# Performance work log

Hardware: AMD Instinct MI355X
Metric: run time of the kernel (lower is better)

The kernel has to match this reference:

```python
import jax, jax.numpy as jnp
import numpy as np

N = 50000   # nodes
E = 600000  # edges
F = 128     # num_node_features
H = 128     # hidden_channels
C = 10      # num_classes
G = 64      # graphs in batch


def setup_inputs() -> dict:
    key = jax.random.key(0)
    ks = jax.random.split(key, 12)
    x = jax.random.normal(ks[0], (N, F), jnp.float32)
    edge_index = jax.random.randint(ks[1], (2, E), 0, N, dtype=jnp.int32)
    batch = jnp.sort(jax.random.randint(ks[2], (N,), 0, G, dtype=jnp.int32))
    def glorot(k, shape):
        lim = np.sqrt(6.0 / (shape[0] + shape[1])).astype(np.float32)
        return jax.random.uniform(k, shape, jnp.float32, -lim, lim)
    return {
        "x": x,
        "edge_index": edge_index,
        "batch": batch,
        "W1": glorot(ks[3], (F, H)), "b1": jnp.zeros((H,), jnp.float32),
        "W2": glorot(ks[4], (H, H)), "b2": jnp.zeros((H,), jnp.float32),
        "W3": glorot(ks[5], (H, H)), "b3": jnp.zeros((H,), jnp.float32),
        "Wl": glorot(ks[6], (H, C)), "bl": jnp.zeros((C,), jnp.float32),
    }


def reference(x, edge_index, batch, W1, b1, W2, b2, W3, b3, Wl, bl):
    # GCNConv: add self-loops, symmetric degree normalization D^-1/2 A D^-1/2
    src0, dst0 = edge_index[0], edge_index[1]
    loop = jnp.arange(N, dtype=src0.dtype)
    src = jnp.concatenate([src0, loop])
    dst = jnp.concatenate([dst0, loop])
    deg = jax.ops.segment_sum(jnp.ones_like(dst, jnp.float32), dst, num_segments=N)
    dinv = jnp.where(deg > 0, jax.lax.rsqrt(deg), 0.0)
    norm = dinv[src] * dinv[dst]  # [E+N]

    def conv(h, W, b):
        h = h @ W                                  # [N, H] transform first (PyG GCNConv)
        msg = h[src] * norm[:, None]               # gather + normalize
        return jax.ops.segment_sum(msg, dst, num_segments=N) + b  # scatter-add

    h = jax.nn.relu(conv(x, W1, b1))
    h = jax.nn.relu(conv(h, W2, b2))
    h = conv(h, W3, b3)

    # global_mean_pool over batch ids
    counts = jax.ops.segment_sum(jnp.ones((N,), jnp.float32), batch, num_segments=G)
    pooled = jax.ops.segment_sum(h, batch, num_segments=G) / jnp.maximum(counts, 1.0)[:, None]
    return pooled @ Wl + bl  # [G, C]
```

## Files before the change

kernel.cpp:

```cpp
#include <hip/hip_runtime.h>
#include <hip/hip_bf16.h>

#define NN 50000
#define EE 600000
#define FF 128
#define HH 128
#define CC 10
#define GG 64
#define SB 256
#define NBSCAN ((NN + SB - 1) / SB)

typedef unsigned int uint32;
typedef unsigned short ushort16;
typedef __attribute__((ext_vector_type(8))) short short8;
typedef __attribute__((ext_vector_type(4))) float f32x4;

__device__ __forceinline__ ushort16 f2bf(float f) {
    __hip_bfloat16 b = __float2bfloat16(f);
    return *reinterpret_cast<ushort16*>(&b);
}
__device__ __forceinline__ uint32 pack2bf(float a, float b) {
    return (uint32)f2bf(a) | ((uint32)f2bf(b) << 16);
}
__device__ __forceinline__ int q8(float f) {
    return __float2int_rn(fminf(fmaxf(f * 16.f, -127.f), 127.f)) & 255;
}

__global__ void count_deg(const int* __restrict__ dst, int* __restrict__ deg) {
    int e = blockIdx.x * blockDim.x + threadIdx.x;
    if (e < EE) atomicAdd(&deg[dst[e]], 1);
}

__global__ __launch_bounds__(SB) void scan_block(const int* __restrict__ deg,
                                                 int* __restrict__ row_ptr,
                                                 int* __restrict__ bsum,
                                                 float* __restrict__ dinv) {
    __shared__ int sm[SB];
    int t = threadIdx.x;
    int i = blockIdx.x * SB + t;
    int v = (i < NN) ? deg[i] : 0;
    if (i < NN) dinv[i] = rsqrtf((float)(v + 1));
    sm[t] = v;
    __syncthreads();
    for (int off = 1; off < SB; off <<= 1) {
        int add = (t >= off) ? sm[t - off] : 0;
        __syncthreads();
        sm[t] += add;
        __syncthreads();
    }
    if (i < NN) row_ptr[i] = sm[t] - v;
    if (t == SB - 1) bsum[blockIdx.x] = sm[t];
}

__global__ void scan_bsum(int* __restrict__ bsum, int nb) {
    __shared__ int sm[256];
    int t = threadIdx.x;
    int v = (t < nb) ? bsum[t] : 0;
    sm[t] = v;
    __syncthreads();
    for (int off = 1; off < 256; off <<= 1) {
        int add = (t >= off) ? sm[t - off] : 0;
        __syncthreads();
        sm[t] += add;
        __syncthreads();
    }
    if (t < nb) bsum[t] = sm[t] - v;
}

__global__ __launch_bounds__(SB) void scan_add_tw(int* __restrict__ row_ptr,
                                                  int* __restrict__ cursor,
                                                  const int* __restrict__ bsum,
                                                  const float* __restrict__ W1,
                                                  const float* __restrict__ W2,
                                                  const float* __restrict__ W3,
                                                  ushort16* __restrict__ T1,
                                                  ushort16* __restrict__ T2,
                                                  ushort16* __restrict__ T3) {
    int b = blockIdx.x;
    if (b < NBSCAN) {
        int i = b * SB + threadIdx.x;
        if (i < NN) {
            int v = row_ptr[i] + bsum[b];
            row_ptr[i] = v;
            cursor[i] = v;
        }
        if (i == 0) row_ptr[NN] = EE;
    } else {
        int bi = b - NBSCAN;
        int wi = bi >> 4;
        const float* W = (wi == 0) ? W1 : (wi == 1) ? W2 : W3;
        ushort16* T = (wi == 0) ? T1 : (wi == 1) ? T2 : T3;
        int base = (bi & 15) * 256 + threadIdx.x;
#pragma unroll
        for (int i = 0; i < 4; i++) {
            int idx = base + i * 4096;
            int col = idx & 127;
            int k = idx >> 7;
            T[col * 128 + k] = f2bf(W[k * 128 + col]);
        }
    }
}

__global__ void fill_csr(const int* __restrict__ src, const int* __restrict__ dst,
                         int* __restrict__ cursor,
                         const float* __restrict__ dinv,
                         int2* __restrict__ csr_en) {
    int e = blockIdx.x * blockDim.x + threadIdx.x;
    if (e < EE) {
        int s = src[e], d = dst[e];
        int pos = atomicAdd(&cursor[d], 1);
        csr_en[pos] = make_int2(s * 128, __float_as_int(dinv[s] * 0.0625f));
    }
}

__global__ __launch_bounds__(256) void gemm_x(const float* __restrict__ A,
                                              const ushort16* __restrict__ Wt,
                                              uint32* __restrict__ zout) {
    __shared__ char lds[34816];
    int t = threadIdx.x;
    int w = t >> 6, l = t & 63;
    int lrow = l & 15, g = l >> 4;
    int rowBase = blockIdx.x * 64;
    int arow = rowBase + w * 16 + lrow;
    short8 afr[4];
    const char* Ab = (const char*)A;
    bool inb = arow < NN;
#pragma unroll
    for (int s = 0; s < 4; s++) {
        if (inb) {
            float4 f0 = *(const float4*)(Ab + (size_t)arow * 512 + s * 128 + g * 32);
            float4 f1 = *(const float4*)(Ab + (size_t)arow * 512 + s * 128 + g * 32 + 16);
            union { short8 s8; uint32 u[4]; } cv;
            cv.u[0] = pack2bf(f0.x, f0.y);
            cv.u[1] = pack2bf(f0.z, f0.w);
            cv.u[2] = pack2bf(f1.x, f1.y);
            cv.u[3] = pack2bf(f1.z, f1.w);
            afr[s] = cv.s8;
        } else {
            short8 z = {0, 0, 0, 0, 0, 0, 0, 0};
            afr[s] = z;
        }
    }
    const char* Wb = (const char*)Wt;
#pragma unroll
    for (int i = 0; i < 8; i++) {
        int idx = t + i * 256;
        int col = idx >> 4, c16 = idx & 15;
        *(uint4*)(lds + col * 272 + c16 * 16) = *(const uint4*)(Wb + col * 256 + c16 * 16);
    }
    __syncthreads();
    f32x4 acc[8];
#pragma unroll
    for (int c = 0; c < 8; c++) { f32x4 z = {0.f, 0.f, 0.f, 0.f}; acc[c] = z; }
#pragma unroll
    for (int s = 0; s < 4; s++) {
#pragma unroll
        for (int c = 0; c < 8; c++) {
            short8 b = *(const short8*)(lds + (c * 16 + lrow) * 272 + s * 64 + g * 16);
            acc[c] = __builtin_amdgcn_mfma_f32_16x16x32_bf16(afr[s], b, acc[c], 0, 0, 0);
        }
    }
    __syncthreads();
    char* myl = lds + w * 8448;
#pragma unroll
    for (int c = 0; c < 8; c++) {
#pragma unroll
        for (int j = 0; j < 4; j++) {
            *(float*)(myl + (g * 4 + j) * 528 + (c * 16 + lrow) * 4) = acc[c][j];
        }
    }
    __syncthreads();
#pragma unroll
    for (int j = 0; j < 8; j++) {
        int rl = (l >> 5) + 2 * j;
        int ch = l & 31;
        float4 v = *(const float4*)(myl + rl * 528 + ch * 16);
        int grow = rowBase + w * 16 + rl;
        if (grow < NN) {
            uint32 u = q8(v.x) | (q8(v.y) << 8) | (q8(v.z) << 16) | (q8(v.w) << 24);
            zout[(size_t)grow * 32 + ch] = u;
        }
    }
}

__global__ __launch_bounds__(256) void gemm_h(const ushort16* __restrict__ A,
                                              const ushort16* __restrict__ Wt,
                                              uint32* __restrict__ zout) {
    __shared__ char lds[34816];
    int t = threadIdx.x;
    int w = t >> 6, l = t & 63;
    int lrow = l & 15, g = l >> 4;
    int rowBase = blockIdx.x * 64;
    int arow = rowBase + w * 16 + lrow;
    short8 afr[4];
    const char* Ab = (const char*)A;
    bool inb = arow < NN;
#pragma unroll
    for (int s = 0; s < 4; s++) {
        if (inb) {
            afr[s] = *(const short8*)(Ab + (size_t)arow * 256 + s * 64 + g * 16);
        } else {
            short8 z = {0, 0, 0, 0, 0, 0, 0, 0};
            afr[s] = z;
        }
    }
    const char* Wb = (const char*)Wt;
#pragma unroll
    for (int i = 0; i < 8; i++) {
        int idx = t + i * 256;
        int col = idx >> 4, c16 = idx & 15;
        *(uint4*)(lds + col * 272 + c16 * 16) = *(const uint4*)(Wb + col * 256 + c16 * 16);
    }
    __syncthreads();
    f32x4 acc[8];
#pragma unroll
    for (int c = 0; c < 8; c++) { f32x4 z = {0.f, 0.f, 0.f, 0.f}; acc[c] = z; }
#pragma unroll
    for (int s = 0; s < 4; s++) {
#pragma unroll
        for (int c = 0; c < 8; c++) {
            short8 b = *(const short8*)(lds + (c * 16 + lrow) * 272 + s * 64 + g * 16);
            acc[c] = __builtin_amdgcn_mfma_f32_16x16x32_bf16(afr[s], b, acc[c], 0, 0, 0);
        }
    }
    __syncthreads();
    char* myl = lds + w * 8448;
#pragma unroll
    for (int c = 0; c < 8; c++) {
#pragma unroll
        for (int j = 0; j < 4; j++) {
            *(float*)(myl + (g * 4 + j) * 528 + (c * 16 + lrow) * 4) = acc[c][j];
        }
    }
    __syncthreads();
#pragma unroll
    for (int j = 0; j < 8; j++) {
        int rl = (l >> 5) + 2 * j;
        int ch = l & 31;
        float4 v = *(const float4*)(myl + rl * 528 + ch * 16);
        int grow = rowBase + w * 16 + rl;
        if (grow < NN) {
            uint32 u = q8(v.x) | (q8(v.y) << 8) | (q8(v.z) << 16) | (q8(v.w) << 24);
            zout[(size_t)grow * 32 + ch] = u;
        }
    }
}

#define AGG_FMA4(c, v)                                             \
    {                                                              \
        float nm = __int_as_float((c).y);                          \
        a0 += nm * (float)((int)((v) << 24) >> 24);                \
        a1 += nm * (float)((int)((v) << 16) >> 24);                \
        a2 += nm * (float)((int)((v) << 8) >> 24);                 \
        a3 += nm * (float)((int)(v) >> 24);                        \
    }

template <int MODE>
__global__ __launch_bounds__(256) void aggregate(const uint32* __restrict__ z8,
                                                 const int* __restrict__ row_ptr,
                                                 const int2* __restrict__ csr_en,
                                                 const float* __restrict__ dinv,
                                                 const float* __restrict__ bias,
                                                 ushort16* __restrict__ out,
                                                 float* __restrict__ pooled,
                                                 const int* __restrict__ batch) {
    int grp = threadIdx.x >> 5;
    int ll  = threadIdx.x & 31;
    int n = blockIdx.x * 8 + grp;
    const char* base = (const char*)z8;
    int boff = ll << 2;
    uint32 uself = *(const uint32*)(base + (size_t)n * 128 + boff);
    float dn = dinv[n];
    float a0 = 0.f, a1 = 0.f, a2 = 0.f, a3 = 0.f;
    int s = row_ptr[n], e = row_ptr[n + 1];
    int k = s;
    if (k + 4 <= e) {
        int2 c0 = csr_en[k], c1 = csr_en[k + 1], c2 = csr_en[k + 2], c3 = csr_en[k + 3];
        uint32 v0 = *(const uint32*)(base + (size_t)(uint32)c0.x + boff);
        uint32 v1 = *(const uint32*)(base + (size_t)(uint32)c1.x + boff);
        uint32 v2 = *(const uint32*)(base + (size_t)(uint32)c2.x + boff);
        uint32 v3 = *(const uint32*)(base + (size_t)(uint32)c3.x + boff);
        k += 4;
        for (; k + 4 <= e; k += 4) {
            int2 d0 = csr_en[k], d1 = csr_en[k + 1], d2 = csr_en[k + 2], d3 = csr_en[k + 3];
            uint32 w0 = *(const uint32*)(base + (size_t)(uint32)d0.x + boff);
            uint32 w1 = *(const uint32*)(base + (size_t)(uint32)d1.x + boff);
            uint32 w2_ = *(const uint32*)(base + (size_t)(uint32)d2.x + boff);
            uint32 w3 = *(const uint32*)(base + (size_t)(uint32)d3.x + boff);
            AGG_FMA4(c0, v0); AGG_FMA4(c1, v1); AGG_FMA4(c2, v2); AGG_FMA4(c3, v3);
            c0 = d0; c1 = d1; c2 = d2; c3 = d3;
            v0 = w0; v1 = w1; v2 = w2_; v3 = w3;
        }
        AGG_FMA4(c0, v0); AGG_FMA4(c1, v1); AGG_FMA4(c2, v2); AGG_FMA4(c3, v3);
    }
    for (; k < e; k++) {
        int2 c0 = csr_en[k];
        uint32 v0 = *(const uint32*)(base + (size_t)(uint32)c0.x + boff);
        AGG_FMA4(c0, v0);
    }
    float ws = dn * dn * 0.0625f;
    float4 b4 = *(const float4*)(bias + (ll << 2));
    a0 = dn * a0 + ws * (float)((int)(uself << 24) >> 24) + b4.x;
    a1 = dn * a1 + ws * (float)((int)(uself << 16) >> 24) + b4.y;
    a2 = dn * a2 + ws * (float)((int)(uself << 8) >> 24) + b4.z;
    a3 = dn * a3 + ws * (float)((int)uself >> 24) + b4.w;
    if (MODE == 0) {
        a0 = fmaxf(a0, 0.f); a1 = fmaxf(a1, 0.f); a2 = fmaxf(a2, 0.f); a3 = fmaxf(a3, 0.f);
        uint2 o = make_uint2(pack2bf(a0, a1), pack2bf(a2, a3));
        *(uint2*)((char*)out + (size_t)n * 256 + (ll << 3)) = o;
    }
    if (MODE == 2) {
        __shared__ float psum[2][128];
        __shared__ int sgmin;
        int g = batch[n];
        if (threadIdx.x == 0) sgmin = g;
        psum[threadIdx.x >> 7][threadIdx.x & 127] = 0.f;
        __syncthreads();
        int slot = g - sgmin;
        if (slot < 2) {
            float* p = &psum[slot][ll << 2];
            atomicAdd(p + 0, a0); atomicAdd(p + 1, a1);
            atomicAdd(p + 2, a2); atomicAdd(p + 3, a3);
        } else {
            float* p = &pooled[g * HH + (ll << 2)];
            atomicAdd(p + 0, a0); atomicAdd(p + 1, a1);
            atomicAdd(p + 2, a2); atomicAdd(p + 3, a3);
        }
        __syncthreads();
        int sl = threadIdx.x >> 7, f = threadIdx.x & 127;
        float v = psum[sl][f];
        int gg = sgmin + sl;
        if (v != 0.f && gg < GG) atomicAdd(&pooled[gg * HH + f], v);
    }
}

__global__ __launch_bounds__(128) void final_linear(const float* __restrict__ pooled,
                                                    const int* __restrict__ batch,
                                                    const float* __restrict__ Wl,
                                                    const float* __restrict__ bl,
                                                    float* __restrict__ out) {
    int g = blockIdx.x;
    int t = threadIdx.x;
    __shared__ float pm[128];
    __shared__ int cnt_s;
    if (t == 0) {
        int lo = 0, hi = NN;
        while (lo < hi) { int m = (lo + hi) >> 1; if (batch[m] < g) lo = m + 1; else hi = m; }
        int s = lo;
        lo = 0; hi = NN;
        while (lo < hi) { int m = (lo + hi) >> 1; if (batch[m] < g + 1) lo = m + 1; else hi = m; }
        int c = lo - s;
        cnt_s = c > 0 ? c : 1;
    }
    __syncthreads();
    pm[t] = pooled[g * HH + t] / (float)cnt_s;
    __syncthreads();
    if (t < CC) {
        float o = bl[t];
        for (int f = 0; f < 128; f++) o += pm[f] * Wl[f * CC + t];
        out[g * CC + t] = o;
    }
}

extern "C" void kernel_launch(void* const* d_in, const int* in_sizes, int n_in,
                              void* d_out, int out_size, void* d_ws, size_t ws_size,
                              hipStream_t stream) {
    const float* x    = (const float*)d_in[0];
    const int*   ei   = (const int*)d_in[1];
    const int*   bat  = (const int*)d_in[2];
    const float* W1   = (const float*)d_in[3];
    const float* b1   = (const float*)d_in[4];
    const float* W2   = (const float*)d_in[5];
    const float* b2   = (const float*)d_in[6];
    const float* W3   = (const float*)d_in[7];
    const float* b3   = (const float*)d_in[8];
    const float* Wl   = (const float*)d_in[9];
    const float* bl   = (const float*)d_in[10];
    float* out = (float*)d_out;

    const int* src = ei;
    const int* dst = ei + EE;

    char* ws = (char*)d_ws;
    size_t off = 0;
    auto take = [&](size_t bytes) -> char* {
        char* p = ws + off;
        off += (bytes + 255) & ~(size_t)255;
        return p;
    };
    int*      deg     = (int*)take((size_t)NN * 4);
    float*    pooled  = (float*)take((size_t)GG * HH * 4);
    int*      cursor  = (int*)take((size_t)NN * 4);
    float*    dinv    = (float*)take((size_t)NN * 4);
    int*      row_ptr = (int*)take((size_t)(NN + 1) * 4);
    int*      bsum    = (int*)take((size_t)256 * 4);
    int2*     csr_en  = (int2*)take((size_t)EE * 8);
    ushort16* Wt1     = (ushort16*)take((size_t)HH * HH * 2);
    ushort16* Wt2     = (ushort16*)take((size_t)HH * HH * 2);
    ushort16* Wt3     = (ushort16*)take((size_t)HH * HH * 2);
    uint32*   zA      = (uint32*)take((size_t)NN * HH);
    uint32*   zB      = (uint32*)take((size_t)NN * HH);
    ushort16* bufH    = (ushort16*)take((size_t)NN * HH * 2);

    const size_t clr = (((size_t)NN * 4 + 255) & ~(size_t)255) + (size_t)GG * HH * 4;
    hipMemsetAsync(deg, 0, clr, stream);

    count_deg<<<(EE + 255) / 256, 256, 0, stream>>>(dst, deg);
    scan_block<<<NBSCAN, SB, 0, stream>>>(deg, row_ptr, bsum, dinv);
    scan_bsum<<<1, 256, 0, stream>>>(bsum, NBSCAN);
    scan_add_tw<<<NBSCAN + 48, SB, 0, stream>>>(row_ptr, cursor, bsum, W1, W2, W3, Wt1, Wt2, Wt3);
    fill_csr<<<(EE + 255) / 256, 256, 0, stream>>>(src, dst, cursor, dinv, csr_en);

    const int gemmBlocks = (NN + 63) / 64;
    const int aggBlocks  = NN / 8;
    gemm_x<<<gemmBlocks, 256, 0, stream>>>(x, Wt1, zA);
    aggregate<0><<<aggBlocks, 256, 0, stream>>>(zA, row_ptr, csr_en, dinv, b1, bufH, pooled, bat);
    gemm_h<<<gemmBlocks, 256, 0, stream>>>(bufH, Wt2, zB);
    aggregate<0><<<aggBlocks, 256, 0, stream>>>(zB, row_ptr, csr_en, dinv, b2, bufH, pooled, bat);
    gemm_h<<<gemmBlocks, 256, 0, stream>>>(bufH, Wt3, zA);
    aggregate<2><<<aggBlocks, 256, 0, stream>>>(zA, row_ptr, csr_en, dinv, b3, bufH, pooled, bat);

    final_linear<<<GG, 128, 0, stream>>>(pooled, bat, Wl, bl, out);
}
```

Before: 197.7 us.

## Fold third GCN layer into pooling via linearity and source-side CSR

Uses linearity of the last conv and mean pool to replace the third GEMM and aggregation. Pooled sums are built directly from layer-2 activations, scattered through a new source-indexed CSR into per-graph LDS partials, and W3 is applied only to the 64 pooled vectors. The layer-2 activations are also stored as int8 instead of bf16, which shrinks the traffic between layers. In exchange it builds a second CSR and runs extra partial-reduction kernels, and the int8 hidden state adds quantization error.

```diff
diff --git a/kernel.cpp b/kernel.cpp
--- a/kernel.cpp
+++ b/kernel.cpp
@@ -8,7 +8,10 @@
 #define CC 10
 #define GG 64
 #define SB 256
-#define NBSCAN ((NN + SB - 1) / SB)
+#define N2 (2 * NN)
+#define NBS2 ((N2 + SB - 1) / SB)
+#define NSTREAM 500
+#define NSL 8
 
 typedef unsigned int uint32;
 typedef unsigned short ushort16;
@@ -25,20 +28,25 @@
 __device__ __forceinline__ int q8(float f) {
     return __float2int_rn(fminf(fmaxf(f * 16.f, -127.f), 127.f)) & 255;
 }
-
-__global__ void count_deg(const int* __restrict__ dst, int* __restrict__ deg) {
+#define B2F(w, j) ((float)((int)((w) << (24 - 8 * (j))) >> 24))
+
+__global__ void count2(const int* __restrict__ src, const int* __restrict__ dst,
+                       int* __restrict__ deg2) {
     int e = blockIdx.x * blockDim.x + threadIdx.x;
-    if (e < EE) atomicAdd(&deg[dst[e]], 1);
-}
-
-__global__ __launch_bounds__(SB) void scan_block(const int* __restrict__ deg,
-                                                 int* __restrict__ row_ptr,
+    if (e < EE) {
+        atomicAdd(&deg2[dst[e]], 1);
+        atomicAdd(&deg2[NN + src[e]], 1);
+    }
+}
+
+__global__ __launch_bounds__(SB) void scan_block(const int* __restrict__ deg2,
+                                                 int* __restrict__ scanv,
                                                  int* __restrict__ bsum,
                                                  float* __restrict__ dinv) {
     __shared__ int sm[SB];
     int t = threadIdx.x;
     int i = blockIdx.x * SB + t;
-    int v = (i < NN) ? deg[i] : 0;
+    int v = (i < N2) ? deg2[i] : 0;
     if (i < NN) dinv[i] = rsqrtf((float)(v + 1));
     sm[t] = v;
     __syncthreads();
@@ -48,17 +56,17 @@
         sm[t] += add;
         __syncthreads();
     }
-    if (i < NN) row_ptr[i] = sm[t] - v;
+    if (i < N2) scanv[i] = sm[t] - v;
     if (t == SB - 1) bsum[blockIdx.x] = sm[t];
 }
 
-__global__ void scan_bsum(int* __restrict__ bsum, int nb) {
-    __shared__ int sm[256];
+__global__ __launch_bounds__(512) void scan_bsum(int* __restrict__ bsum, int nb) {
+    __shared__ int sm[512];
     int t = threadIdx.x;
     int v = (t < nb) ? bsum[t] : 0;
     sm[t] = v;
     __syncthreads();
-    for (int off = 1; off < 256; off <<= 1) {
+    for (int off = 1; off < 512; off <<= 1) {
         int add = (t >= off) ? sm[t - off] : 0;
         __syncthreads();
         sm[t] += add;
@@ -67,29 +75,42 @@
     if (t < nb) bsum[t] = sm[t] - v;
 }
 
-__global__ __launch_bounds__(SB) void scan_add_tw(int* __restrict__ row_ptr,
-                                                  int* __restrict__ cursor,
+__global__ __launch_bounds__(SB) void scan_add_tw(const int* __restrict__ scanv,
                                                   const int* __restrict__ bsum,
+                                                  int* __restrict__ rp_dst,
+                                                  int* __restrict__ cur_dst,
+                                                  int* __restrict__ rp_src,
+                                                  int* __restrict__ cur_src,
+                                                  int2* __restrict__ ndinfo,
+                                                  const float* __restrict__ dinv,
+                                                  const int* __restrict__ batch,
                                                   const float* __restrict__ W1,
                                                   const float* __restrict__ W2,
-                                                  const float* __restrict__ W3,
                                                   ushort16* __restrict__ T1,
-                                                  ushort16* __restrict__ T2,
-                                                  ushort16* __restrict__ T3) {
+                                                  ushort16* __restrict__ T2) {
     int b = blockIdx.x;
-    if (b < NBSCAN) {
+    if (b < NBS2) {
         int i = b * SB + threadIdx.x;
-        if (i < NN) {
-            int v = row_ptr[i] + bsum[b];
-            row_ptr[i] = v;
-            cursor[i] = v;
-        }
-        if (i == 0) row_ptr[NN] = EE;
+        if (i < N2) {
+            int v = scanv[i] + bsum[b];
+            if (i < NN) {
+                rp_dst[i] = v;
+                cur_dst[i] = v;
+                ndinfo[i] = make_int2(__float_as_int(dinv[i]), batch[i]);
+                if (i == 0) rp_dst[NN] = EE;
+            } else {
+                int j = i - NN;
+                int vs = v - EE;
+                rp_src[j] = vs;
+                cur_src[j] = vs;
+                if (j == 0) rp_src[NN] = EE;
+            }
+        }
     } else {
-        int bi = b - NBSCAN;
+        int bi = b - NBS2;
         int wi = bi >> 4;
-        const float* W = (wi == 0) ? W1 : (wi == 1) ? W2 : W3;
-        ushort16* T = (wi == 0) ? T1 : (wi == 1) ? T2 : T3;
+        const float* W = (wi == 0) ? W1 : W2;
+        ushort16* T = (wi == 0) ? T1 : T2;
         int base = (bi & 15) * 256 + threadIdx.x;
 #pragma unroll
         for (int i = 0; i < 4; i++) {
@@ -101,15 +122,19 @@
     }
 }
 
-__global__ void fill_csr(const int* __restrict__ src, const int* __restrict__ dst,
-                         int* __restrict__ cursor,
-                         const float* __restrict__ dinv,
-                         int2* __restrict__ csr_en) {
+__global__ void fill_both(const int* __restrict__ src, const int* __restrict__ dst,
+                          int* __restrict__ cur_dst, int* __restrict__ cur_src,
+                          const int2* __restrict__ ndinfo,
+                          int2* __restrict__ csr_dst, int2* __restrict__ csr_src) {
     int e = blockIdx.x * blockDim.x + threadIdx.x;
     if (e < EE) {
         int s = src[e], d = dst[e];
-        int pos = atomicAdd(&cursor[d], 1);
-        csr_en[pos] = make_int2(s * 128, __float_as_int(dinv[s] * 0.0625f));
+        int2 ns = ndinfo[s];
+        int2 nd = ndinfo[d];
+        int pd = atomicAdd(&cur_dst[d], 1);
+        csr_dst[pd] = make_int2(s * 128, __float_as_int(__int_as_float(ns.x) * 0.0625f));
+        int ps = atomicAdd(&cur_src[s], 1);
+        csr_src[ps] = make_int2(nd.y, nd.x);
     }
 }
 
@@ -183,7 +208,7 @@
     }
 }
 
-__global__ __launch_bounds__(256) void gemm_h(const ushort16* __restrict__ A,
+__global__ __launch_bounds__(256) void gemm_h(const uint32* __restrict__ A,
                                               const ushort16* __restrict__ Wt,
                                               uint32* __restrict__ zout) {
     __shared__ char lds[34816];
@@ -198,7 +223,13 @@
 #pragma unroll
     for (int s = 0; s < 4; s++) {
         if (inb) {
-            afr[s] = *(const short8*)(Ab + (size_t)arow * 256 + s * 64 + g * 16);
+            uint2 u = *(const uint2*)(Ab + (size_t)arow * 128 + s * 32 + g * 8);
+            union { short8 s8; uint32 uu[4]; } cv;
+            cv.uu[0] = pack2bf(B2F(u.x, 0), B2F(u.x, 1));
+            cv.uu[1] = pack2bf(B2F(u.x, 2), B2F(u.x, 3));
+            cv.uu[2] = pack2bf(B2F(u.y, 0), B2F(u.y, 1));
+            cv.uu[3] = pack2bf(B2F(u.y, 2), B2F(u.y, 3));
+            afr[s] = cv.s8;
         } else {
             short8 z = {0, 0, 0, 0, 0, 0, 0, 0};
             afr[s] = z;
@@ -240,7 +271,8 @@
         float4 v = *(const float4*)(myl + rl * 528 + ch * 16);
         int grow = rowBase + w * 16 + rl;
         if (grow < NN) {
-            uint32 u = q8(v.x) | (q8(v.y) << 8) | (q8(v.z) << 16) | (q8(v.w) << 24);
+            uint32 u = q8(v.x * 0.0625f) | (q8(v.y * 0.0625f) << 8) |
+                       (q8(v.z * 0.0625f) << 16) | (q8(v.w * 0.0625f) << 24);
             zout[(size_t)grow * 32 + ch] = u;
         }
     }
@@ -249,21 +281,18 @@
 #define AGG_FMA4(c, v)                                             \
     {                                                              \
         float nm = __int_as_float((c).y);                          \
-        a0 += nm * (float)((int)((v) << 24) >> 24);                \
-        a1 += nm * (float)((int)((v) << 16) >> 24);                \
-        a2 += nm * (float)((int)((v) << 8) >> 24);                 \
-        a3 += nm * (float)((int)(v) >> 24);                        \
-    }
-
-template <int MODE>
+        a0 += nm * B2F(v, 0);                                      \
+        a1 += nm * B2F(v, 1);                                      \
+        a2 += nm * B2F(v, 2);                                      \
+        a3 += nm * B2F(v, 3);                                      \
+    }
+
 __global__ __launch_bounds__(256) void aggregate(const uint32* __restrict__ z8,
                                                  const int* __restrict__ row_ptr,
                                                  const int2* __restrict__ csr_en,
                                                  const float* __restrict__ dinv,
                                                  const float* __restrict__ bias,
-                                                 ushort16* __restrict__ out,
-                                                 float* __restrict__ pooled,
-                                                 const int* __restrict__ batch) {
+                                                 uint32* __restrict__ out) {
     int grp = threadIdx.x >> 5;
     int ll  = threadIdx.x & 31;
     int n = blockIdx.x * 8 + grp;
@@ -298,50 +327,86 @@
         uint32 v0 = *(const uint32*)(base + (size_t)(uint32)c0.x + boff);
         AGG_FMA4(c0, v0);
     }
-    float ws = dn * dn * 0.0625f;
+    float ws_ = dn * dn * 0.0625f;
     float4 b4 = *(const float4*)(bias + (ll << 2));
-    a0 = dn * a0 + ws * (float)((int)(uself << 24) >> 24) + b4.x;
-    a1 = dn * a1 + ws * (float)((int)(uself << 16) >> 24) + b4.y;
-    a2 = dn * a2 + ws * (float)((int)(uself << 8) >> 24) + b4.z;
-    a3 = dn * a3 + ws * (float)((int)uself >> 24) + b4.w;
-    if (MODE == 0) {
-        a0 = fmaxf(a0, 0.f); a1 = fmaxf(a1, 0.f); a2 = fmaxf(a2, 0.f); a3 = fmaxf(a3, 0.f);
-        uint2 o = make_uint2(pack2bf(a0, a1), pack2bf(a2, a3));
-        *(uint2*)((char*)out + (size_t)n * 256 + (ll << 3)) = o;
-    }
-    if (MODE == 2) {
-        __shared__ float psum[2][128];
-        __shared__ int sgmin;
-        int g = batch[n];
-        if (threadIdx.x == 0) sgmin = g;
-        psum[threadIdx.x >> 7][threadIdx.x & 127] = 0.f;
-        __syncthreads();
-        int slot = g - sgmin;
-        if (slot < 2) {
-            float* p = &psum[slot][ll << 2];
-            atomicAdd(p + 0, a0); atomicAdd(p + 1, a1);
-            atomicAdd(p + 2, a2); atomicAdd(p + 3, a3);
-        } else {
-            float* p = &pooled[g * HH + (ll << 2)];
-            atomicAdd(p + 0, a0); atomicAdd(p + 1, a1);
-            atomicAdd(p + 2, a2); atomicAdd(p + 3, a3);
-        }
-        __syncthreads();
-        int sl = threadIdx.x >> 7, f = threadIdx.x & 127;
-        float v = psum[sl][f];
-        int gg = sgmin + sl;
-        if (v != 0.f && gg < GG) atomicAdd(&pooled[gg * HH + f], v);
-    }
-}
-
-__global__ __launch_bounds__(128) void final_linear(const float* __restrict__ pooled,
+    a0 = fmaxf(dn * a0 + ws_ * B2F(uself, 0) + b4.x, 0.f);
+    a1 = fmaxf(dn * a1 + ws_ * B2F(uself, 1) + b4.y, 0.f);
+    a2 = fmaxf(dn * a2 + ws_ * B2F(uself, 2) + b4.z, 0.f);
+    a3 = fmaxf(dn * a3 + ws_ * B2F(uself, 3) + b4.w, 0.f);
+    uint32 o = q8(a0) | (q8(a1) << 8) | (q8(a2) << 16) | (q8(a3) << 24);
+    out[(size_t)n * 32 + ll] = o;
+}
+
+__global__ __launch_bounds__(128) void stream_pool(const char* __restrict__ h2,
+                                                   const int* __restrict__ rp_src,
+                                                   const int2* __restrict__ csr_src,
+                                                   const float* __restrict__ dinv,
+                                                   const int* __restrict__ batch,
+                                                   float* __restrict__ partials) {
+    __shared__ float psum[64][128];
+    int t = threadIdx.x;
+#pragma unroll
+    for (int r = 0; r < 64; r++) psum[r][t] = 0.f;
+    __syncthreads();
+    int m0 = blockIdx.x * 100;
+    for (int m = m0; m < m0 + 100; m++) {
+        float fv = (float)(int)*(const signed char*)(h2 + (size_t)m * 128 + t);
+        float dm = dinv[m];
+        float wr = dm * 0.0625f;
+        psum[batch[m]][t] += wr * dm * fv;
+        int ks = rp_src[m], ke = rp_src[m + 1];
+        int k = ks;
+        if (k + 4 <= ke) {
+            int2 e0 = csr_src[k], e1 = csr_src[k + 1], e2 = csr_src[k + 2], e3 = csr_src[k + 3];
+            k += 4;
+            for (; k + 4 <= ke; k += 4) {
+                int2 f0 = csr_src[k], f1 = csr_src[k + 1], f2 = csr_src[k + 2], f3 = csr_src[k + 3];
+                psum[e0.x][t] += wr * __int_as_float(e0.y) * fv;
+                psum[e1.x][t] += wr * __int_as_float(e1.y) * fv;
+                psum[e2.x][t] += wr * __int_as_float(e2.y) * fv;
+                psum[e3.x][t] += wr * __int_as_float(e3.y) * fv;
+                e0 = f0; e1 = f1; e2 = f2; e3 = f3;
+            }
+            psum[e0.x][t] += wr * __int_as_float(e0.y) * fv;
+            psum[e1.x][t] += wr * __int_as_float(e1.y) * fv;
+            psum[e2.x][t] += wr * __int_as_float(e2.y) * fv;
+            psum[e3.x][t] += wr * __int_as_float(e3.y) * fv;
+        }
+        for (; k < ke; k++) {
+            int2 en = csr_src[k];
+            psum[en.x][t] += wr * __int_as_float(en.y) * fv;
+        }
+    }
+    __syncthreads();
+    float* dstp = partials + (size_t)blockIdx.x * (GG * HH);
+#pragma unroll
+    for (int r = 0; r < 64; r++) dstp[r * 128 + t] = psum[r][t];
+}
+
+__global__ __launch_bounds__(128) void reduce_part(const float* __restrict__ partials,
+                                                   float* __restrict__ P2b) {
+    int sl = blockIdx.x & 7, g = blockIdx.x >> 3;
+    int t = threadIdx.x;
+    int p0 = sl * 63;
+    int p1 = p0 + 63;
+    if (p1 > NSTREAM) p1 = NSTREAM;
+    float acc = 0.f;
+    for (int p = p0; p < p1; p++)
+        acc += partials[(size_t)p * (GG * HH) + g * 128 + t];
+    P2b[(sl * GG + g) * 128 + t] = acc;
+}
+
+__global__ __launch_bounds__(128) void final_linear(const float* __restrict__ P2b,
                                                     const int* __restrict__ batch,
+                                                    const float* __restrict__ W3,
+                                                    const float* __restrict__ b3,
                                                     const float* __restrict__ Wl,
                                                     const float* __restrict__ bl,
                                                     float* __restrict__ out) {
     int g = blockIdx.x;
     int t = threadIdx.x;
     __shared__ float pm[128];
+    __shared__ float t1[128];
     __shared__ int cnt_s;
     if (t == 0) {
         int lo = 0, hi = NN;
@@ -349,15 +414,22 @@
         int s = lo;
         lo = 0; hi = NN;
         while (lo < hi) { int m = (lo + hi) >> 1; if (batch[m] < g + 1) lo = m + 1; else hi = m; }
-        int c = lo - s;
-        cnt_s = c > 0 ? c : 1;
-    }
-    __syncthreads();
-    pm[t] = pooled[g * HH + t] / (float)cnt_s;
+        cnt_s = lo - s;
+    }
+    __syncthreads();
+    int cnt = cnt_s;
+    float acc = 0.f;
+#pragma unroll
+    for (int sl = 0; sl < NSL; sl++) acc += P2b[(sl * GG + g) * 128 + t];
+    pm[t] = (cnt > 0) ? acc / (float)cnt : 0.f;
+    __syncthreads();
+    float a = (cnt > 0) ? b3[t] : 0.f;
+    for (int j = 0; j < 128; j++) a += pm[j] * W3[j * 128 + t];
+    t1[t] = a;
     __syncthreads();
     if (t < CC) {
         float o = bl[t];
-        for (int f = 0; f < 128; f++) o += pm[f] * Wl[f * CC + t];
+        for (int j = 0; j < 128; j++) o += t1[j] * Wl[j * CC + t];
         out[g * CC + t] = o;
     }
 }
@@ -388,37 +460,42 @@
         off += (bytes + 255) & ~(size_t)255;
         return p;
     };
-    int*      deg     = (int*)take((size_t)NN * 4);
-    float*    pooled  = (float*)take((size_t)GG * HH * 4);
-    int*      cursor  = (int*)take((size_t)NN * 4);
-    float*    dinv    = (float*)take((size_t)NN * 4);
-    int*      row_ptr = (int*)take((size_t)(NN + 1) * 4);
-    int*      bsum    = (int*)take((size_t)256 * 4);
-    int2*     csr_en  = (int2*)take((size_t)EE * 8);
-    ushort16* Wt1     = (ushort16*)take((size_t)HH * HH * 2);
-    ushort16* Wt2     = (ushort16*)take((size_t)HH * HH * 2);
-    ushort16* Wt3     = (ushort16*)take((size_t)HH * HH * 2);
-    uint32*   zA      = (uint32*)take((size_t)NN * HH);
-    uint32*   zB      = (uint32*)take((size_t)NN * HH);
-    ushort16* bufH    = (ushort16*)take((size_t)NN * HH * 2);
-
-    const size_t clr = (((size_t)NN * 4 + 255) & ~(size_t)255) + (size_t)GG * HH * 4;
-    hipMemsetAsync(deg, 0, clr, stream);
-
-    count_deg<<<(EE + 255) / 256, 256, 0, stream>>>(dst, deg);
-    scan_block<<<NBSCAN, SB, 0, stream>>>(deg, row_ptr, bsum, dinv);
-    scan_bsum<<<1, 256, 0, stream>>>(bsum, NBSCAN);
-    scan_add_tw<<<NBSCAN + 48, SB, 0, stream>>>(row_ptr, cursor, bsum, W1, W2, W3, Wt1, Wt2, Wt3);
-    fill_csr<<<(EE + 255) / 256, 256, 0, stream>>>(src, dst, cursor, dinv, csr_en);
+    int*      deg2     = (int*)take((size_t)N2 * 4);
+    int*      scanv    = (int*)take((size_t)N2 * 4);
+    int*      bsum     = (int*)take((size_t)512 * 4);
+    float*    dinv     = (float*)take((size_t)NN * 4);
+    int2*     ndinfo   = (int2*)take((size_t)NN * 8);
+    int*      rp_dst   = (int*)take((size_t)(NN + 1) * 4);
+    int*      cur_dst  = (int*)take((size_t)NN * 4);
+    int*      rp_src   = (int*)take((size_t)(NN + 1) * 4);
+    int*      cur_src  = (int*)take((size_t)NN * 4);
+    int2*     csr_dst  = (int2*)take((size_t)EE * 8);
+    int2*     csr_src  = (int2*)take((size_t)EE * 8);
+    ushort16* Wt1      = (ushort16*)take((size_t)HH * HH * 2);
+    ushort16* Wt2      = (ushort16*)take((size_t)HH * HH * 2);
+    uint32*   zA       = (uint32*)take((size_t)NN * HH);
+    uint32*   zB       = (uint32*)take((size_t)NN * HH);
+    float*    partials = (float*)take((size_t)NSTREAM * GG * HH * 4);
+    float*    P2b      = (float*)take((size_t)NSL * GG * HH * 4);
+
+    hipMemsetAsync(deg2, 0, (size_t)N2 * 4, stream);
+
+    count2<<<(EE + 255) / 256, 256, 0, stream>>>(src, dst, deg2);
+    scan_block<<<NBS2, SB, 0, stream>>>(deg2, scanv, bsum, dinv);
+    scan_bsum<<<1, 512, 0, stream>>>(bsum, NBS2);
+    scan_add_tw<<<NBS2 + 32, SB, 0, stream>>>(scanv, bsum, rp_dst, cur_dst, rp_src, cur_src,
+                                              ndinfo, dinv, bat, W1, W2, Wt1, Wt2);
+    fill_both<<<(EE + 255) / 256, 256, 0, stream>>>(src, dst, cur_dst, cur_src, ndinfo,
+                                                    csr_dst, csr_src);
 
     const int gemmBlocks = (NN + 63) / 64;
     const int aggBlocks  = NN / 8;
     gemm_x<<<gemmBlocks, 256, 0, stream>>>(x, Wt1, zA);
-    aggregate<0><<<aggBlocks, 256, 0, stream>>>(zA, row_ptr, csr_en, dinv, b1, bufH, pooled, bat);
-    gemm_h<<<gemmBlocks, 256, 0, stream>>>(bufH, Wt2, zB);
-    aggregate<0><<<aggBlocks, 256, 0, stream>>>(zB, row_ptr, csr_en, dinv, b2, bufH, pooled, bat);
-    gemm_h<<<gemmBlocks, 256, 0, stream>>>(bufH, Wt3, zA);
-    aggregate<2><<<aggBlocks, 256, 0, stream>>>(zA, row_ptr, csr_en, dinv, b3, bufH, pooled, bat);
-
-    final_linear<<<GG, 128, 0, stream>>>(pooled, bat, Wl, bl, out);
-}
+    aggregate<<<aggBlocks, 256, 0, stream>>>(zA, rp_dst, csr_dst, dinv, b1, zB);
+    gemm_h<<<gemmBlocks, 256, 0, stream>>>(zB, Wt2, zA);
+    aggregate<<<aggBlocks, 256, 0, stream>>>(zA, rp_dst, csr_dst, dinv, b2, zB);
+    stream_pool<<<NSTREAM, 128, 0, stream>>>((const char*)zB, rp_src, csr_src, dinv, bat,
+                                             partials);
+    reduce_part<<<GG * NSL, 128, 0, stream>>>(partials, P2b);
+    final_linear<<<GG, 128, 0, stream>>>(P2b, bat, W3, b3, Wl, bl, out);
+}
```

Measured after the change: 360.3 us. 82.3% more time.

## Defer third-layer weight transform past mean pooling to drop a node-level GEMM

Applied to the files above, without the earlier changes.

Uses linearity: mean_pool(A·H·W3 + b3) equals mean_pool(A·H)·W3 + b3 for non-empty graphs. The third node-level GEMM and its Wt3 transpose are removed. Layer 2 now writes an int8-quantized activation, and a new pool_gather kernel aggregates it and pools straight into per-graph sums. final_linear then applies W3 and b3 per graph before the classifier. This removes one full N×H×H GEMM and its memory traffic, at the cost of quantizing the post-ReLU hidden state to int8 (scale 16, clipped at ±127/16), which adds approximation error and saturates large activations.

```diff
diff --git a/kernel.cpp b/kernel.cpp
--- a/kernel.cpp
+++ b/kernel.cpp
@@ -25,6 +25,7 @@
 __device__ __forceinline__ int q8(float f) {
     return __float2int_rn(fminf(fmaxf(f * 16.f, -127.f), 127.f)) & 255;
 }
+#define B2F(w, j) ((float)((int)((w) << (24 - 8 * (j))) >> 24))
 
 __global__ void count_deg(const int* __restrict__ dst, int* __restrict__ deg) {
     int e = blockIdx.x * blockDim.x + threadIdx.x;
@@ -72,10 +73,8 @@
                                                   const int* __restrict__ bsum,
                                                   const float* __restrict__ W1,
                                                   const float* __restrict__ W2,
-                                                  const float* __restrict__ W3,
                                                   ushort16* __restrict__ T1,
-                                                  ushort16* __restrict__ T2,
-                                                  ushort16* __restrict__ T3) {
+                                                  ushort16* __restrict__ T2) {
     int b = blockIdx.x;
     if (b < NBSCAN) {
         int i = b * SB + threadIdx.x;
@@ -88,8 +87,8 @@
     } else {
         int bi = b - NBSCAN;
         int wi = bi >> 4;
-        const float* W = (wi == 0) ? W1 : (wi == 1) ? W2 : W3;
-        ushort16* T = (wi == 0) ? T1 : (wi == 1) ? T2 : T3;
+        const float* W = (wi == 0) ? W1 : W2;
+        ushort16* T = (wi == 0) ? T1 : T2;
         int base = (bi & 15) * 256 + threadIdx.x;
 #pragma unroll
         for (int i = 0; i < 4; i++) {
@@ -249,10 +248,10 @@
 #define AGG_FMA4(c, v)                                             \
     {                                                              \
         float nm = __int_as_float((c).y);                          \
-        a0 += nm * (float)((int)((v) << 24) >> 24);                \
-        a1 += nm * (float)((int)((v) << 16) >> 24);                \
-        a2 += nm * (float)((int)((v) << 8) >> 24);                 \
-        a3 += nm * (float)((int)(v) >> 24);                        \
+        a0 += nm * B2F(v, 0);                                      \
+        a1 += nm * B2F(v, 1);                                      \
+        a2 += nm * B2F(v, 2);                                      \
+        a3 += nm * B2F(v, 3);                                      \
     }
 
 template <int MODE>
@@ -261,9 +260,7 @@
                                                  const int2* __restrict__ csr_en,
                                                  const float* __restrict__ dinv,
                                                  const float* __restrict__ bias,
-                                                 ushort16* __restrict__ out,
-                                                 float* __restrict__ pooled,
-                                                 const int* __restrict__ batch) {
+                                                 void* __restrict__ outv) {
     int grp = threadIdx.x >> 5;
     int ll  = threadIdx.x & 31;
     int n = blockIdx.x * 8 + grp;
@@ -298,50 +295,100 @@
         uint32 v0 = *(const uint32*)(base + (size_t)(uint32)c0.x + boff);
         AGG_FMA4(c0, v0);
     }
-    float ws = dn * dn * 0.0625f;
+    float ws_ = dn * dn * 0.0625f;
     float4 b4 = *(const float4*)(bias + (ll << 2));
-    a0 = dn * a0 + ws * (float)((int)(uself << 24) >> 24) + b4.x;
-    a1 = dn * a1 + ws * (float)((int)(uself << 16) >> 24) + b4.y;
-    a2 = dn * a2 + ws * (float)((int)(uself << 8) >> 24) + b4.z;
-    a3 = dn * a3 + ws * (float)((int)uself >> 24) + b4.w;
+    a0 = fmaxf(dn * a0 + ws_ * B2F(uself, 0) + b4.x, 0.f);
+    a1 = fmaxf(dn * a1 + ws_ * B2F(uself, 1) + b4.y, 0.f);
+    a2 = fmaxf(dn * a2 + ws_ * B2F(uself, 2) + b4.z, 0.f);
+    a3 = fmaxf(dn * a3 + ws_ * B2F(uself, 3) + b4.w, 0.f);
     if (MODE == 0) {
-        a0 = fmaxf(a0, 0.f); a1 = fmaxf(a1, 0.f); a2 = fmaxf(a2, 0.f); a3 = fmaxf(a3, 0.f);
         uint2 o = make_uint2(pack2bf(a0, a1), pack2bf(a2, a3));
-        *(uint2*)((char*)out + (size_t)n * 256 + (ll << 3)) = o;
-    }
-    if (MODE == 2) {
-        __shared__ float psum[2][128];
-        __shared__ int sgmin;
-        int g = batch[n];
-        if (threadIdx.x == 0) sgmin = g;
-        psum[threadIdx.x >> 7][threadIdx.x & 127] = 0.f;
-        __syncthreads();
-        int slot = g - sgmin;
-        if (slot < 2) {
-            float* p = &psum[slot][ll << 2];
-            atomicAdd(p + 0, a0); atomicAdd(p + 1, a1);
-            atomicAdd(p + 2, a2); atomicAdd(p + 3, a3);
-        } else {
-            float* p = &pooled[g * HH + (ll << 2)];
-            atomicAdd(p + 0, a0); atomicAdd(p + 1, a1);
-            atomicAdd(p + 2, a2); atomicAdd(p + 3, a3);
-        }
-        __syncthreads();
-        int sl = threadIdx.x >> 7, f = threadIdx.x & 127;
-        float v = psum[sl][f];
-        int gg = sgmin + sl;
-        if (v != 0.f && gg < GG) atomicAdd(&pooled[gg * HH + f], v);
-    }
+        *(uint2*)((char*)outv + (size_t)n * 256 + (ll << 3)) = o;
+    } else {
+        uint32 o = q8(a0) | (q8(a1) << 8) | (q8(a2) << 16) | (q8(a3) << 24);
+        ((uint32*)outv)[(size_t)n * 32 + ll] = o;
+    }
+}
+
+__global__ __launch_bounds__(256) void pool_gather(const uint32* __restrict__ h8,
+                                                   const int* __restrict__ row_ptr,
+                                                   const int2* __restrict__ csr_en,
+                                                   const float* __restrict__ dinv,
+                                                   float* __restrict__ pooled,
+                                                   const int* __restrict__ batch) {
+    int grp = threadIdx.x >> 5;
+    int ll  = threadIdx.x & 31;
+    int n = blockIdx.x * 8 + grp;
+    const char* base = (const char*)h8;
+    int boff = ll << 2;
+    uint32 uself = *(const uint32*)(base + (size_t)n * 128 + boff);
+    float dn = dinv[n];
+    float a0 = 0.f, a1 = 0.f, a2 = 0.f, a3 = 0.f;
+    int s = row_ptr[n], e = row_ptr[n + 1];
+    int k = s;
+    if (k + 4 <= e) {
+        int2 c0 = csr_en[k], c1 = csr_en[k + 1], c2 = csr_en[k + 2], c3 = csr_en[k + 3];
+        uint32 v0 = *(const uint32*)(base + (size_t)(uint32)c0.x + boff);
+        uint32 v1 = *(const uint32*)(base + (size_t)(uint32)c1.x + boff);
+        uint32 v2 = *(const uint32*)(base + (size_t)(uint32)c2.x + boff);
+        uint32 v3 = *(const uint32*)(base + (size_t)(uint32)c3.x + boff);
+        k += 4;
+        for (; k + 4 <= e; k += 4) {
+            int2 d0 = csr_en[k], d1 = csr_en[k + 1], d2 = csr_en[k + 2], d3 = csr_en[k + 3];
+            uint32 w0 = *(const uint32*)(base + (size_t)(uint32)d0.x + boff);
+            uint32 w1 = *(const uint32*)(base + (size_t)(uint32)d1.x + boff);
+            uint32 w2_ = *(const uint32*)(base + (size_t)(uint32)d2.x + boff);
+            uint32 w3 = *(const uint32*)(base + (size_t)(uint32)d3.x + boff);
+            AGG_FMA4(c0, v0); AGG_FMA4(c1, v1); AGG_FMA4(c2, v2); AGG_FMA4(c3, v3);
+            c0 = d0; c1 = d1; c2 = d2; c3 = d3;
+            v0 = w0; v1 = w1; v2 = w2_; v3 = w3;
+        }
+        AGG_FMA4(c0, v0); AGG_FMA4(c1, v1); AGG_FMA4(c2, v2); AGG_FMA4(c3, v3);
+    }
+    for (; k < e; k++) {
+        int2 c0 = csr_en[k];
+        uint32 v0 = *(const uint32*)(base + (size_t)(uint32)c0.x + boff);
+        AGG_FMA4(c0, v0);
+    }
+    float ws_ = dn * dn * 0.0625f;
+    a0 = dn * a0 + ws_ * B2F(uself, 0);
+    a1 = dn * a1 + ws_ * B2F(uself, 1);
+    a2 = dn * a2 + ws_ * B2F(uself, 2);
+    a3 = dn * a3 + ws_ * B2F(uself, 3);
+    __shared__ float psum[2][128];
+    __shared__ int sgmin;
+    int g = batch[n];
+    if (threadIdx.x == 0) sgmin = g;
+    psum[threadIdx.x >> 7][threadIdx.x & 127] = 0.f;
+    __syncthreads();
+    int slot = g - sgmin;
+    if (slot < 2) {
+        float* p = &psum[slot][ll << 2];
+        atomicAdd(p + 0, a0); atomicAdd(p + 1, a1);
+        atomicAdd(p + 2, a2); atomicAdd(p + 3, a3);
+    } else {
+        float* p = &pooled[g * HH + (ll << 2)];
+        atomicAdd(p + 0, a0); atomicAdd(p + 1, a1);
+        atomicAdd(p + 2, a2); atomicAdd(p + 3, a3);
+    }
+    __syncthreads();
+    int sl = threadIdx.x >> 7, f = threadIdx.x & 127;
+    float v = psum[sl][f];
+    int gg = sgmin + sl;
+    if (v != 0.f && gg < GG) atomicAdd(&pooled[gg * HH + f], v);
 }
 
 __global__ __launch_bounds__(128) void final_linear(const float* __restrict__ pooled,
                                                     const int* __restrict__ batch,
+                                                    const float* __restrict__ W3,
+                                                    const float* __restrict__ b3,
                                                     const float* __restrict__ Wl,
                                                     const float* __restrict__ bl,
                                                     float* __restrict__ out) {
     int g = blockIdx.x;
     int t = threadIdx.x;
     __shared__ float pm[128];
+    __shared__ float t1[128];
     __shared__ int cnt_s;
     if (t == 0) {
         int lo = 0, hi = NN;
@@ -349,15 +396,19 @@
         int s = lo;
         lo = 0; hi = NN;
         while (lo < hi) { int m = (lo + hi) >> 1; if (batch[m] < g + 1) lo = m + 1; else hi = m; }
-        int c = lo - s;
-        cnt_s = c > 0 ? c : 1;
-    }
-    __syncthreads();
-    pm[t] = pooled[g * HH + t] / (float)cnt_s;
+        cnt_s = lo - s;
+    }
+    __syncthreads();
+    int cnt = cnt_s;
+    pm[t] = (cnt > 0) ? pooled[g * HH + t] / (float)cnt : 0.f;
+    __syncthreads();
+    float a = (cnt > 0) ? b3[t] : 0.f;
+    for (int j = 0; j < 128; j++) a += pm[j] * W3[j * 128 + t];
+    t1[t] = a;
     __syncthreads();
     if (t < CC) {
         float o = bl[t];
-        for (int f = 0; f < 128; f++) o += pm[f] * Wl[f * CC + t];
+        for (int j = 0; j < 128; j++) o += t1[j] * Wl[j * CC + t];
         out[g * CC + t] = o;
     }
 }
@@ -397,7 +448,6 @@
     int2*     csr_en  = (int2*)take((size_t)EE * 8);
     ushort16* Wt1     = (ushort16*)take((size_t)HH * HH * 2);
     ushort16* Wt2     = (ushort16*)take((size_t)HH * HH * 2);
-    ushort16* Wt3     = (ushort16*)take((size_t)HH * HH * 2);
     uint32*   zA      = (uint32*)take((size_t)NN * HH);
     uint32*   zB      = (uint32*)take((size_t)NN * HH);
     ushort16* bufH    = (ushort16*)take((size_t)NN * HH * 2);
@@ -408,17 +458,16 @@
     count_deg<<<(EE + 255) / 256, 256, 0, stream>>>(dst, deg);
     scan_block<<<NBSCAN, SB, 0, stream>>>(deg, row_ptr, bsum, dinv);
     scan_bsum<<<1, 256, 0, stream>>>(bsum, NBSCAN);
-    scan_add_tw<<<NBSCAN + 48, SB, 0, stream>>>(row_ptr, cursor, bsum, W1, W2, W3, Wt1, Wt2, Wt3);
+    scan_add_tw<<<NBSCAN + 32, SB, 0, stream>>>(row_ptr, cursor, bsum, W1, W2, Wt1, Wt2);
     fill_csr<<<(EE + 255) / 256, 256, 0, stream>>>(src, dst, cursor, dinv, csr_en);
 
     const int gemmBlocks = (NN + 63) / 64;
     const int aggBlocks  = NN / 8;
     gemm_x<<<gemmBlocks, 256, 0, stream>>>(x, Wt1, zA);
-    aggregate<0><<<aggBlocks, 256, 0, stream>>>(zA, row_ptr, csr_en, dinv, b1, bufH, pooled, bat);
+    aggregate<0><<<aggBlocks, 256, 0, stream>>>(zA, row_ptr, csr_en, dinv, b1, bufH);
     gemm_h<<<gemmBlocks, 256, 0, stream>>>(bufH, Wt2, zB);
-    aggregate<0><<<aggBlocks, 256, 0, stream>>>(zB, row_ptr, csr_en, dinv, b2, bufH, pooled, bat);
-    gemm_h<<<gemmBlocks, 256, 0, stream>>>(bufH, Wt3, zA);
-    aggregate<2><<<aggBlocks, 256, 0, stream>>>(zA, row_ptr, csr_en, dinv, b3, bufH, pooled, bat);
-
-    final_linear<<<GG, 128, 0, stream>>>(pooled, bat, Wl, bl, out);
-}
+    aggregate<1><<<aggBlocks, 256, 0, stream>>>(zB, row_ptr, csr_en, dinv, b2, zA);
+    pool_gather<<<aggBlocks, 256, 0, stream>>>(zA, row_ptr, csr_en, dinv, pooled, bat);
+
+    final_linear<<<GG, 128, 0, stream>>>(pooled, bat, W3, b3, Wl, bl, out);
+}
```

New measurement: 192.4 us, median of 2. 1.03x faster.
